# Kernel optimization log

Hardware: AMD Instinct MI355X
Metric: run time of the kernel (lower is better)

## Reference

```python
import jax, jax.numpy as jnp
import numpy as np

B, N, IN, HD, NH, L, OUT = 256, 128, 9, 128, 8, 4, 60
DH = HD // NH
ALPHA = 0.6
EPS = 1e-5

def _ln(x, g, b):
    m = jnp.mean(x, axis=-1, keepdims=True)
    v = jnp.mean((x - m) ** 2, axis=-1, keepdims=True)
    return (x - m) * jax.lax.rsqrt(v + EPS) * g + b

def setup_inputs():
    key = jax.random.key(0)
    ks = jax.random.split(key, 30)
    p = lambda i, s: jax.random.normal(ks[i], s, jnp.float32) * 0.02
    strong = (jax.random.uniform(ks[25], (N, N)) < 0.15).astype(jnp.float32)
    strong = jnp.maximum(strong, jnp.eye(N, dtype=jnp.float32))  # self loops
    weak_mask = (jax.random.uniform(ks[26], (N, N)) < 0.10).astype(jnp.float32)
    return {
        'x': jax.random.normal(ks[0], (B, N, IN), jnp.float32),
        'conv_w': p(1, (HD, IN)), 'conv_b': p(2, (HD,)),
        'bn_gamma': jnp.ones((HD,), jnp.float32), 'bn_beta': jnp.zeros((HD,), jnp.float32),
        'bn_mean': jnp.zeros((HD,), jnp.float32), 'bn_var': jnp.ones((HD,), jnp.float32),
        'W': p(3, (L, HD, HD)), 'a_src': p(4, (L, NH, DH)), 'a_dst': p(5, (L, NH, DH)),
        'ln_g': jnp.ones((L, HD), jnp.float32), 'ln_b': jnp.zeros((L, HD), jnp.float32),
        'ffn_w1': p(6, (L, HD, 2 * HD)), 'ffn_b1': p(7, (L, 2 * HD)),
        'ffn_w2': p(8, (L, 2 * HD, HD)), 'ffn_b2': p(9, (L, HD)),
        'norm_g': jnp.ones((HD,), jnp.float32), 'norm_b': jnp.zeros((HD,), jnp.float32),
        'proj_w': p(10, (HD, HD)), 'proj_b': p(11, (HD,)),
        'head_w1': p(12, (HD, HD // 2)), 'head_b1': p(13, (HD // 2,)),
        'head_w2': p(14, (HD // 2, OUT)), 'head_b2': p(15, (OUT,)),
        'strong_adj': strong, 'weak_mask': weak_mask,
        'weak_param': p(16, (N, N)), 'edge_weight_adj': p(17, (N, N)),
    }

def reference(x, conv_w, conv_b, bn_gamma, bn_beta, bn_mean, bn_var, W, a_src, a_dst, ln_g, ln_b, ffn_w1, ffn_b1, ffn_w2, ffn_b2, norm_g, norm_b, proj_w, proj_b, head_w1, head_b1, head_w2, head_b2, strong_adj, weak_mask, weak_param, edge_weight_adj):
    # embedding: Conv1d(k=1) == per-node linear, then eval-mode BatchNorm1d + ReLU
    h = jnp.einsum('bni,oi->bno', x, conv_w) + conv_b  # [B,N,HD]
    h = (h - bn_mean) * jax.lax.rsqrt(bn_var + EPS) * bn_gamma + bn_beta
    h = jax.nn.relu(h)
    # weak adjacency: learnable gated edges, row-normalized (shared across layers)
    Aw = jax.nn.sigmoid(weak_param) * weak_mask
    Aw = Aw / (jnp.sum(Aw, axis=-1, keepdims=True) + EPS)  # [N,N]
    for i in range(L):
        res = h
        hp = jnp.einsum('bnd,de->bne', h, W[i]).reshape(B, N, NH, DH)
        s = jnp.einsum('bnhd,hd->bnh', hp, a_src[i])
        t = jnp.einsum('bnhd,hd->bnh', hp, a_dst[i])
        e = jax.nn.leaky_relu(s[:, :, None, :] + t[:, None, :, :], 0.2)  # [B,N,N,H]
        e = e + edge_weight_adj[None, :, :, None]  # learned per-edge bias
        e = jnp.where(strong_adj[None, :, :, None] > 0, e, jnp.float32(-1e9))
        att = jax.nn.softmax(e, axis=2)  # softmax over neighbors j
        strong_out = jnp.einsum('bijh,bjhd->bihd', att, hp)
        weak_out = jnp.einsum('ij,bjhd->bihd', Aw, hp)
        g = jax.nn.relu(ALPHA * strong_out + (1.0 - ALPHA) * weak_out).reshape(B, N, HD)
        g = _ln(g, ln_g[i], ln_b[i])
        g = jax.nn.relu(g @ ffn_w1[i] + ffn_b1[i]) @ ffn_w2[i] + ffn_b2[i]
        h = g + res
    h = _ln(h, norm_g, norm_b)
    h = h @ proj_w + proj_b
    h = jnp.mean(h, axis=1)  # mean-pool over nodes -> [B,HD]
    h = jax.nn.relu(h @ head_w1 + head_b1)
    return h @ head_w2 + head_b2  # [B,OUT]
```

## Files before the change

kernel.cpp:

```cpp
#include <hip/hip_runtime.h>
#include <hip/hip_bf16.h>

typedef __hip_bfloat16 bf16;
typedef unsigned short u16;
typedef __attribute__((ext_vector_type(8))) short bfrag;
typedef __attribute__((ext_vector_type(4))) float cfrag;

union BF { bfrag v; u16 u[8]; unsigned w[4]; };
union CF { cfrag v; float f[4]; };

#define MFMA(a,b,c) __builtin_amdgcn_mfma_f32_16x16x32_bf16(a,b,c,0,0,0)

#define BB   256
#define NN   128
#define IND  9
#define HDD  128
#define LLY  4
#define OUTD 60
#define LOG2E 1.44269504f

__device__ __forceinline__ float b2f(bf16 v){ return __bfloat162float(v); }
__device__ __forceinline__ float u2f(u16 u){ return __uint_as_float(((unsigned)u) << 16); }
__device__ __forceinline__ u16 f2bf_bits(float f){
    unsigned u = __float_as_uint(f);
    return (u16)((u + 0x7FFFu + ((u >> 16) & 1u)) >> 16);
}
__device__ __forceinline__ unsigned pk2(float a, float b){
    union { __hip_bfloat162 h; unsigned u; } c;
    c.h = __float22bfloat162_rn(make_float2(a, b));
    return c.u;
}
__device__ __forceinline__ float wave_sum(float v){
    #pragma unroll
    for (int m = 32; m; m >>= 1) v += __shfl_xor(v, m, 64);
    return v;
}
__device__ __forceinline__ float ldin(const void* p, int i, bool isbf){
    return isbf ? b2f(((const bf16*)p)[i]) : ((const float*)p)[i];
}

struct SrcPtrs { const void* p[28]; };

__device__ const int NCV_OFF[19] = {0,1152,1280,1408,1536,1664,1792,2304,2816,3840,
                                    4352,4480,4608,20992,21120,29312,29376,33216,33276};
__device__ const int NCV_SRC[18] = {1,2,3,4,5,6,10,11,13,15,16,17,18,19,20,21,22,23};

__global__ __launch_bounds__(256) void k_prep(
    SrcPtrs S, float* __restrict__ pf,
    u16* __restrict__ WT, u16* __restrict__ w1T, u16* __restrict__ w2T,
    u16* __restrict__ WAb, u16* __restrict__ ew2, u16* __restrict__ Aw16,
    int* __restrict__ flagOut)
{
    const unsigned* xw = (const unsigned*)S.p[0];
    int lane = threadIdx.x & 63;
    int cnt = 0;
    for (int i = lane; i < 512; i += 64) {
        float v = __uint_as_float((xw[i] & 0xFFFFu) << 16);
        if (!(fabsf(v) < 32.f)) cnt++;
    }
    bool isbf = wave_sum((float)cnt) < 16.f;
    if (blockIdx.x == 0 && threadIdx.x == 0) *flagOut = isbf ? 1 : 0;

    int blk = blockIdx.x, tid = threadIdx.x;
    if (blk < 131) {
        int idx = blk * 256 + tid;
        if (idx < 33276) {
            int y = 17;
            #pragma unroll 1
            for (int t = 1; t < 18; t++) if (idx < NCV_OFF[t]) { y = t - 1; break; }
            pf[idx] = ldin(S.p[NCV_SRC[y]], idx - NCV_OFF[y], isbf);
        }
    } else if (blk < 387) {
        int j = (blk - 131) * 256 + tid;
        int l = j >> 14, r = j & 16383, n = r >> 7, k = r & 127;
        WT[j] = f2bf_bits(ldin(S.p[7], (l << 14) + k * 128 + n, isbf));
    } else if (blk < 899) {
        int j = (blk - 387) * 256 + tid;
        int l = j >> 15, r = j & 32767, n = r >> 7, k = r & 127;
        w1T[j] = f2bf_bits(ldin(S.p[12], (l << 15) + k * 256 + n, isbf));
    } else if (blk < 1411) {
        int j = (blk - 899) * 256 + tid;
        int l = j >> 15, r = j & 32767, n = r >> 8, k = r & 255;
        w2T[j] = f2bf_bits(ldin(S.p[14], (l << 15) + k * 128 + n, isbf));
    } else if (blk < 1443) {
        int j = (blk - 1411) * 256 + tid;
        int l = j >> 11, r = j & 2047, n = r >> 7, k = r & 127;
        int h = n & 7;
        const void* ap = (n < 8) ? S.p[8] : S.p[9];
        float sacc = 0.f;
        #pragma unroll 1
        for (int d = 0; d < 16; d++)
            sacc += ldin(S.p[7], l * 16384 + k * 128 + h * 16 + d, isbf)
                  * ldin(ap, l * 128 + h * 16 + d, isbf);
        WAb[j] = f2bf_bits(sacc);
    } else if (blk < 1507) {
        int j = (blk - 1443) * 256 + tid;
        float sav = ldin(S.p[24], j, isbf);
        float ewv = ldin(S.p[27], j, isbf);
        ew2[j] = f2bf_bits(sav > 0.f ? ewv * LOG2E : -1e30f);
    } else {
        __shared__ float red[2];
        int i = blk - 1507, j = tid & 127;
        float v = 0.f;
        if (tid < 128) {
            float wmv = ldin(S.p[25], i * 128 + j, isbf);
            float wpv = ldin(S.p[26], i * 128 + j, isbf);
            v = wmv / (1.f + __expf(-wpv));
            float sm = wave_sum(v);
            if ((tid & 63) == 0) red[tid >> 6] = sm;
        }
        __syncthreads();
        if (tid < 128) {
            float tot = red[0] + red[1];
            Aw16[i * 128 + j] = f2bf_bits(v / (tot + 1e-5f));
        }
    }
}

__global__ __launch_bounds__(256) void k_embed(
    const void* __restrict__ xraw, const int* __restrict__ flag,
    const float* __restrict__ pf,
    float* __restrict__ h, u16* __restrict__ h16, float* __restrict__ pooled)
{
    int b = blockIdx.x, half = blockIdx.y, tid = threadIdx.x;
    bool isbf = (*flag != 0);
    if (half == 0 && tid < 128) pooled[b * 128 + tid] = 0.f;
    int d = tid & 127, nh = tid >> 7;
    float wreg[IND];
    #pragma unroll
    for (int k = 0; k < IND; k++) wreg[k] = pf[d * IND + k];
    float scale = rsqrtf(pf[1664 + d] + 1e-5f) * pf[1280 + d];
    float bias  = pf[1408 + d] - pf[1536 + d] * scale;
    float cbd   = pf[1152 + d];
    #pragma unroll 1
    for (int it = 0; it < 32; it++) {
        int bn = b * NN + half * 64 + it * 2 + nh;
        float acc = cbd;
        #pragma unroll
        for (int k = 0; k < IND; k++) acc = fmaf(ldin(xraw, bn * IND + k, isbf), wreg[k], acc);
        acc = fmaxf(fmaf(acc, scale, bias), 0.f);
        h[bn * HDD + d] = acc;
        h16[bn * HDD + d] = f2bf_bits(acc);
    }
}

__global__ __launch_bounds__(256, 3) void k_layer(
    float* __restrict__ hg, u16* __restrict__ h16g,
    const u16* __restrict__ WT, const u16* __restrict__ WAb,
    const u16* __restrict__ Aw16, const u16* __restrict__ ew2g,
    const float* __restrict__ lng, const float* __restrict__ lnb,
    const u16* __restrict__ w1T, const float* __restrict__ b1,
    const u16* __restrict__ w2T, const float* __restrict__ b2,
    const float* __restrict__ ng, const float* __restrict__ nb,
    float* __restrict__ pooled, int last)
{
    __shared__ __align__(16) u16 hpT[128 * 136];
    __shared__ float st2[2048];
    float* s2 = st2;
    float* t2 = st2 + 1024;
    u16* gbuf = hpT;
    u16* hidb = hpT + 64 * 136;

    const int b = blockIdx.x, half = blockIdx.y;
    const int tid = threadIdx.x, lane = tid & 63, wv = tid >> 6;
    const int l15 = lane & 15, kg = lane >> 4;
    const int wrow = wv * 16;
    const int base = b * NN;

    float lngr[8], lnbr[8], b2r[8];
    #pragma unroll
    for (int nt = 0; nt < 8; nt++) {
        int col = nt * 16 + l15;
        lngr[nt] = lng[col]; lnbr[nt] = lnb[col]; b2r[nt] = b2[col];
    }

    {
        CF acc[2][8], ast[2];
        #pragma unroll
        for (int mt = 0; mt < 2; mt++) {
            #pragma unroll
            for (int r = 0; r < 4; r++) ast[mt].f[r] = 0.f;
            #pragma unroll
            for (int nt = 0; nt < 8; nt++)
                #pragma unroll
                for (int r = 0; r < 4; r++) acc[mt][nt].f[r] = 0.f;
        }
        #pragma unroll 1
        for (int kk = 0; kk < 4; kk++) {
            bfrag af0 = *(const bfrag*)&h16g[(base + wv*32 +      l15) * 128 + kk*32 + kg*8];
            bfrag af1 = *(const bfrag*)&h16g[(base + wv*32 + 16 + l15) * 128 + kk*32 + kg*8];
            bfrag wab = *(const bfrag*)&WAb[l15 * 128 + kk*32 + kg*8];
            ast[0].v = MFMA(af0, wab, ast[0].v);
            ast[1].v = MFMA(af1, wab, ast[1].v);
            #pragma unroll
            for (int nt = 0; nt < 8; nt++) {
                bfrag bw = *(const bfrag*)&WT[(nt*16 + l15) * 128 + kk*32 + kg*8];
                acc[0][nt].v = MFMA(af0, bw, acc[0][nt].v);
                acc[1][nt].v = MFMA(af1, bw, acc[1][nt].v);
            }
        }
        #pragma unroll
        for (int mt = 0; mt < 2; mt++) {
            #pragma unroll
            for (int nt = 0; nt < 8; nt++) {
                int col = nt*16 + l15;
                #pragma unroll
                for (int rp = 0; rp < 2; rp++) {
                    int row = wv*32 + mt*16 + kg*4 + rp*2;
                    *(unsigned*)&hpT[col * 136 + row] =
                        pk2(acc[mt][nt].f[rp*2], acc[mt][nt].f[rp*2+1]);
                }
            }
            #pragma unroll
            for (int r = 0; r < 4; r++) {
                int node = wv*32 + mt*16 + kg*4 + r;
                float v = ast[mt].f[r] * LOG2E;
                float* dst = (l15 < 8) ? &s2[l15 * 128 + node] : &t2[(l15 - 8) * 128 + node];
                *dst = v;
            }
        }
    }
    __syncthreads();

    const int grow = half*64 + wrow + l15;
    CF accW[8];
    #pragma unroll
    for (int nt = 0; nt < 8; nt++)
        #pragma unroll
        for (int r = 0; r < 4; r++) accW[nt].f[r] = 0.f;
    #pragma unroll 1
    for (int kk = 0; kk < 4; kk++) {
        bfrag awf = *(const bfrag*)&Aw16[grow * 128 + kk*32 + kg*8];
        #pragma unroll
        for (int nt = 0; nt < 8; nt++) {
            bfrag hb2 = *(const bfrag*)&hpT[(nt*16 + l15) * 136 + kk*32 + kg*8];
            accW[nt].v = MFMA(awf, hb2, accW[nt].v);
        }
    }

    CF accS[8];
    #pragma unroll
    for (int nt = 0; nt < 8; nt++)
        #pragma unroll
        for (int r = 0; r < 4; r++) accS[nt].f[r] = 0.f;

    float ew2f[4][8];
    #pragma unroll
    for (int kk = 0; kk < 4; kk++) {
        BF e2; e2.v = *(const bfrag*)&ew2g[grow * 128 + kk*32 + kg*8];
        #pragma unroll
        for (int j = 0; j < 8; j++) ew2f[kk][j] = u2f(e2.u[j]);
    }
    #pragma unroll 1
    for (int h = 0; h < 8; h++) {
        bfrag hb[4];
        #pragma unroll
        for (int kk = 0; kk < 4; kk++)
            hb[kk] = *(const bfrag*)&hpT[(h*16 + l15) * 136 + kk*32 + kg*8];
        float sA = s2[h * 128 + grow];
        float pv[4][8];
        float sm = 0.f;
        #pragma unroll
        for (int kk = 0; kk < 4; kk++) {
            const float* tp = &t2[h * 128 + kk*32 + kg*8];
            #pragma unroll
            for (int j = 0; j < 8; j++) {
                float x2 = sA + tp[j];
                float lk = fmaxf(x2, 0.2f * x2);
                float p = __builtin_amdgcn_exp2f(lk + ew2f[kk][j]);
                pv[kk][j] = p; sm += p;
            }
        }
        sm += __shfl_xor(sm, 16, 64);
        sm += __shfl_xor(sm, 32, 64);
        float inv = __builtin_amdgcn_rcpf(sm);
        #pragma unroll
        for (int kk = 0; kk < 4; kk++) {
            BF pb;
            #pragma unroll
            for (int q = 0; q < 4; q++)
                pb.w[q] = pk2(pv[kk][2*q] * inv, pv[kk][2*q+1] * inv);
            accS[h].v = MFMA(pb.v, hb[kk], accS[h].v);
        }
    }

    float gv[8][4];
    #pragma unroll
    for (int nt = 0; nt < 8; nt++)
        #pragma unroll
        for (int r = 0; r < 4; r++)
            gv[nt][r] = fmaxf(0.6f * accS[nt].f[r] + 0.4f * accW[nt].f[r], 0.f);
    u16 gb16[8][4];
    #pragma unroll
    for (int r = 0; r < 4; r++) {
        float s1 = 0.f, sq = 0.f;
        #pragma unroll
        for (int nt = 0; nt < 8; nt++) { float x = gv[nt][r]; s1 += x; sq = fmaf(x, x, sq); }
        #pragma unroll
        for (int m = 1; m <= 8; m <<= 1) { s1 += __shfl_xor(s1, m, 64); sq += __shfl_xor(sq, m, 64); }
        float mu = s1 * (1.f / 128.f);
        float var = sq * (1.f / 128.f) - mu * mu;
        float rs = rsqrtf(fmaxf(var, 0.f) + 1e-5f);
        #pragma unroll
        for (int nt = 0; nt < 8; nt++)
            gb16[nt][r] = f2bf_bits(fmaf((gv[nt][r] - mu) * rs, lngr[nt], lnbr[nt]));
    }
    __syncthreads();
    #pragma unroll
    for (int nt = 0; nt < 8; nt++) {
        int col = nt*16 + l15;
        #pragma unroll
        for (int r = 0; r < 4; r++)
            gbuf[(wrow + kg*4 + r) * 136 + col] = gb16[nt][r];
    }
    __syncthreads();

    CF acc2[8];
    #pragma unroll
    for (int nt = 0; nt < 8; nt++)
        #pragma unroll
        for (int r = 0; r < 4; r++) acc2[nt].f[r] = 0.f;

    #pragma unroll 1
    for (int nh = 0; nh < 2; nh++) {
        float b1r[8];
        #pragma unroll
        for (int nt = 0; nt < 8; nt++) b1r[nt] = b1[nh*128 + nt*16 + l15];
        CF a1[8];
        #pragma unroll
        for (int nt = 0; nt < 8; nt++)
            #pragma unroll
            for (int r = 0; r < 4; r++) a1[nt].f[r] = 0.f;
        #pragma unroll 1
        for (int kk = 0; kk < 4; kk++) {
            bfrag gf = *(const bfrag*)&gbuf[(wrow + l15) * 136 + kk*32 + kg*8];
            #pragma unroll
            for (int nt = 0; nt < 8; nt++) {
                bfrag wf = *(const bfrag*)&w1T[(nh*128 + nt*16 + l15) * 128 + kk*32 + kg*8];
                a1[nt].v = MFMA(gf, wf, a1[nt].v);
            }
        }
        __syncthreads();
        #pragma unroll
        for (int nt = 0; nt < 8; nt++) {
            int col = nt*16 + l15;
            #pragma unroll
            for (int r = 0; r < 4; r++)
                hidb[(wrow + kg*4 + r) * 136 + col] = f2bf_bits(fmaxf(a1[nt].f[r] + b1r[nt], 0.f));
        }
        __syncthreads();
        #pragma unroll 1
        for (int kk = 0; kk < 4; kk++) {
            bfrag hf = *(const bfrag*)&hidb[(wrow + l15) * 136 + kk*32 + kg*8];
            #pragma unroll
            for (int nt = 0; nt < 8; nt++) {
                bfrag wf = *(const bfrag*)&w2T[(nt*16 + l15) * 256 + nh*128 + kk*32 + kg*8];
                acc2[nt].v = MFMA(hf, wf, acc2[nt].v);
            }
        }
    }

    float hv[8][4];
    #pragma unroll
    for (int nt = 0; nt < 8; nt++) {
        #pragma unroll
        for (int r = 0; r < 4; r++) {
            int gi = (base + half*64 + wrow + kg*4 + r) * HDD + nt*16 + l15;
            hv[nt][r] = acc2[nt].f[r] + b2r[nt] + hg[gi];
        }
    }
    if (!last) {
        #pragma unroll
        for (int nt = 0; nt < 8; nt++) {
            #pragma unroll
            for (int r = 0; r < 4; r++) {
                int gi = (base + half*64 + wrow + kg*4 + r) * HDD + nt*16 + l15;
                hg[gi] = hv[nt][r];
                h16g[gi] = f2bf_bits(hv[nt][r]);
            }
        }
    } else {
        float ngr[8], nbr[8];
        #pragma unroll
        for (int nt = 0; nt < 8; nt++) { int col = nt*16 + l15; ngr[nt] = ng[col]; nbr[nt] = nb[col]; }
        float pacc[8];
        #pragma unroll
        for (int nt = 0; nt < 8; nt++) pacc[nt] = 0.f;
        #pragma unroll
        for (int r = 0; r < 4; r++) {
            float s1 = 0.f, sq = 0.f;
            #pragma unroll
            for (int nt = 0; nt < 8; nt++) { float x = hv[nt][r]; s1 += x; sq = fmaf(x, x, sq); }
            #pragma unroll
            for (int m = 1; m <= 8; m <<= 1) { s1 += __shfl_xor(s1, m, 64); sq += __shfl_xor(sq, m, 64); }
            float mu = s1 * (1.f / 128.f);
            float var = sq * (1.f / 128.f) - mu * mu;
            float rs = rsqrtf(fmaxf(var, 0.f) + 1e-5f);
            #pragma unroll
            for (int nt = 0; nt < 8; nt++)
                pacc[nt] += fmaf((hv[nt][r] - mu) * rs, ngr[nt], nbr[nt]);
        }
        __syncthreads();
        float* psum = st2;
        #pragma unroll
        for (int nt = 0; nt < 8; nt++)
            psum[(wv*4 + kg) * 128 + nt*16 + l15] = pacc[nt];
        __syncthreads();
        if (tid < 128) {
            float tot = 0.f;
            #pragma unroll
            for (int i = 0; i < 16; i++) tot += psum[i * 128 + tid];
            atomicAdd(&pooled[b * HDD + tid], tot);
        }
    }
}

__global__ __launch_bounds__(128) void k_head(
    const float* __restrict__ pooled, const float* __restrict__ pf,
    void* __restrict__ outv, const int* __restrict__ flag)
{
    const float* pw  = pf + 4608;
    const float* pb  = pf + 20992;
    const float* hw1 = pf + 21120;
    const float* hb1 = pf + 29312;
    const float* hw2 = pf + 29376;
    const float* hb2 = pf + 33216;
    int b = blockIdx.x, t = threadIdx.x;
    __shared__ float pm[128], pr[128], r1[64];
    pm[t] = pooled[b * HDD + t] * (1.f / 128.f);
    __syncthreads();
    float a = pb[t];
    #pragma unroll 4
    for (int k = 0; k < 128; k++) a = fmaf(pm[k], pw[k * 128 + t], a);
    pr[t] = a;
    __syncthreads();
    if (t < 64) {
        float a1 = hb1[t];
        #pragma unroll 4
        for (int k = 0; k < 128; k++) a1 = fmaf(pr[k], hw1[k * 64 + t], a1);
        r1[t] = fmaxf(a1, 0.f);
    }
    __syncthreads();
    if (t < OUTD) {
        float a2 = hb2[t];
        #pragma unroll 4
        for (int k = 0; k < 64; k++) a2 = fmaf(r1[k], hw2[k * OUTD + t], a2);
        if (*flag) ((bf16*)outv)[b * OUTD + t] = __float2bfloat16(a2);
        else       ((float*)outv)[b * OUTD + t] = a2;
    }
}

extern "C" void kernel_launch(void* const* d_in, const int* in_sizes, int n_in,
                              void* d_out, int out_size, void* d_ws, size_t ws_size,
                              hipStream_t stream)
{
    float* ws = (float*)d_ws;
    float* pf = ws;
    const float* lng  = pf + 1792;
    const float* lnb  = pf + 2304;
    const float* fb1  = pf + 2816;
    const float* fb2  = pf + 3840;
    const float* ng   = pf + 4352;
    const float* nb   = pf + 4480;

    int*   flag   = (int*)(ws + 33280);
    float* h      = ws + 33536;
    float* pooled = h + 4194304;
    u16* h16    = (u16*)(pooled + 32768);
    u16* WT16   = h16 + 4194304;
    u16* w1T16  = WT16 + 65536;
    u16* w2T16  = w1T16 + 131072;
    u16* WAb16  = w2T16 + 131072;
    u16* Aw16   = WAb16 + 8192;
    u16* ew2p   = Aw16 + 16384;

    SrcPtrs S;
    for (int i = 0; i < 28; i++) S.p[i] = d_in[i];

    k_prep<<<1635, 256, 0, stream>>>(S, pf, WT16, w1T16, w2T16, WAb16, ew2p, Aw16, flag);
    k_embed<<<dim3(BB, 2), 256, 0, stream>>>(d_in[0], flag, pf, h, h16, pooled);

    for (int i = 0; i < LLY; i++) {
        k_layer<<<dim3(BB, 2), 256, 0, stream>>>(
            h, h16,
            WT16 + i * 16384, WAb16 + i * 2048,
            Aw16, ew2p,
            lng + i * 128, lnb + i * 128,
            w1T16 + i * 32768, fb1 + i * 256,
            w2T16 + i * 32768, fb2 + i * 128,
            ng, nb, pooled, (i == LLY - 1) ? 1 : 0);
    }

    k_head<<<BB, 128, 0, stream>>>(pooled, pf, d_out, flag);
}
```

Baseline: 393.7 us.

## Fuse embed, all GAT layers and head into one persistent per-graph kernel

Replaces the separate embed, per-layer and head kernels with a single kernel that runs one 512-thread block per graph and keeps the residual stream in registers and LDS across all four layers. This removes the global round-trips of h/h16 between layers, the atomic pooling, and several launches. The attention t-scores are now stored as bf16 in LDS and the edge bias is reloaded from global each head. In exchange, grid parallelism drops from 512 blocks to 256 larger blocks, and the larger LDS footprint may limit occupancy.

```diff
diff --git a/kernel.cpp b/kernel.cpp
--- a/kernel.cpp
+++ b/kernel.cpp
@@ -18,6 +18,7 @@
 #define LLY  4
 #define OUTD 60
 #define LOG2E 1.44269504f
+#define STR  136
 
 __device__ __forceinline__ float b2f(bf16 v){ return __bfloat162float(v); }
 __device__ __forceinline__ float u2f(u16 u){ return __uint_as_float(((unsigned)u) << 16); }
@@ -117,336 +118,315 @@
     }
 }
 
-__global__ __launch_bounds__(256) void k_embed(
+#define LDSB (2*128*STR*2 + 8192)
+__global__ __launch_bounds__(512, 2) void k_net(
     const void* __restrict__ xraw, const int* __restrict__ flag,
     const float* __restrict__ pf,
-    float* __restrict__ h, u16* __restrict__ h16, float* __restrict__ pooled)
+    const u16* __restrict__ WTg, const u16* __restrict__ WAbg,
+    const u16* __restrict__ Awg, const u16* __restrict__ ew2g,
+    const u16* __restrict__ w1Tg, const u16* __restrict__ w2Tg,
+    void* __restrict__ outv)
 {
-    int b = blockIdx.x, half = blockIdx.y, tid = threadIdx.x;
-    bool isbf = (*flag != 0);
-    if (half == 0 && tid < 128) pooled[b * 128 + tid] = 0.f;
-    int d = tid & 127, nh = tid >> 7;
-    float wreg[IND];
-    #pragma unroll
-    for (int k = 0; k < IND; k++) wreg[k] = pf[d * IND + k];
-    float scale = rsqrtf(pf[1664 + d] + 1e-5f) * pf[1280 + d];
-    float bias  = pf[1408 + d] - pf[1536 + d] * scale;
-    float cbd   = pf[1152 + d];
-    #pragma unroll 1
-    for (int it = 0; it < 32; it++) {
-        int bn = b * NN + half * 64 + it * 2 + nh;
-        float acc = cbd;
-        #pragma unroll
-        for (int k = 0; k < IND; k++) acc = fmaf(ldin(xraw, bn * IND + k, isbf), wreg[k], acc);
-        acc = fmaxf(fmaf(acc, scale, bias), 0.f);
-        h[bn * HDD + d] = acc;
-        h16[bn * HDD + d] = f2bf_bits(acc);
-    }
-}
-
-__global__ __launch_bounds__(256, 3) void k_layer(
-    float* __restrict__ hg, u16* __restrict__ h16g,
-    const u16* __restrict__ WT, const u16* __restrict__ WAb,
-    const u16* __restrict__ Aw16, const u16* __restrict__ ew2g,
-    const float* __restrict__ lng, const float* __restrict__ lnb,
-    const u16* __restrict__ w1T, const float* __restrict__ b1,
-    const u16* __restrict__ w2T, const float* __restrict__ b2,
-    const float* __restrict__ ng, const float* __restrict__ nb,
-    float* __restrict__ pooled, int last)
-{
-    __shared__ __align__(16) u16 hpT[128 * 136];
-    __shared__ float st2[2048];
-    float* s2 = st2;
-    float* t2 = st2 + 1024;
-    u16* gbuf = hpT;
-    u16* hidb = hpT + 64 * 136;
-
-    const int b = blockIdx.x, half = blockIdx.y;
+    extern __shared__ __align__(16) char smem[];
+    u16* Abuf = (u16*)smem;
+    u16* Bbuf = Abuf + 128 * STR;
+    float* st2 = (float*)(Bbuf + 128 * STR);
+    float* s2  = st2;
+    u16*   t2u = (u16*)(st2 + 1024);
+
+    const int b = blockIdx.x;
     const int tid = threadIdx.x, lane = tid & 63, wv = tid >> 6;
     const int l15 = lane & 15, kg = lane >> 4;
     const int wrow = wv * 16;
-    const int base = b * NN;
-
-    float lngr[8], lnbr[8], b2r[8];
-    #pragma unroll
-    for (int nt = 0; nt < 8; nt++) {
-        int col = nt * 16 + l15;
-        lngr[nt] = lng[col]; lnbr[nt] = lnb[col]; b2r[nt] = b2[col];
-    }
+    const bool isbf = (*flag != 0);
+
+    float hreg[8][4];
 
     {
-        CF acc[2][8], ast[2];
-        #pragma unroll
-        for (int mt = 0; mt < 2; mt++) {
-            #pragma unroll
-            for (int r = 0; r < 4; r++) ast[mt].f[r] = 0.f;
+        float xr[4][9];
+        #pragma unroll
+        for (int r = 0; r < 4; r++) {
+            int bn = b * NN + wrow + kg * 4 + r;
+            #pragma unroll
+            for (int k = 0; k < IND; k++) xr[r][k] = ldin(xraw, bn * IND + k, isbf);
+        }
+        #pragma unroll 1
+        for (int nt = 0; nt < 8; nt++) {
+            int d = nt * 16 + l15;
+            float cwreg[IND];
+            #pragma unroll
+            for (int k = 0; k < IND; k++) cwreg[k] = pf[d * IND + k];
+            float scale = rsqrtf(pf[1664 + d] + 1e-5f) * pf[1280 + d];
+            float bias  = pf[1408 + d] - pf[1536 + d] * scale;
+            float cbd   = pf[1152 + d];
+            #pragma unroll
+            for (int r = 0; r < 4; r++) {
+                float a = cbd;
+                #pragma unroll
+                for (int k = 0; k < IND; k++) a = fmaf(xr[r][k], cwreg[k], a);
+                a = fmaxf(fmaf(a, scale, bias), 0.f);
+                hreg[nt][r] = a;
+                Abuf[(wrow + kg * 4 + r) * STR + d] = f2bf_bits(a);
+            }
+        }
+    }
+
+    const int arow = wrow + l15;
+
+    #pragma unroll 1
+    for (int l = 0; l < LLY; l++) {
+        const u16* WT  = WTg  + l * 16384;
+        const u16* WAb = WAbg + l * 2048;
+        const u16* w1T = w1Tg + l * 32768;
+        const u16* w2T = w2Tg + l * 32768;
+        const float* fb1 = pf + 2816 + l * 256;
+        const float* fb2 = pf + 3840 + l * 128;
+        const float* lng = pf + 1792 + l * 128;
+        const float* lnb = pf + 2304 + l * 128;
+
+        __syncthreads();
+
+        {
+            CF acc[8], ast;
+            #pragma unroll
+            for (int r = 0; r < 4; r++) ast.f[r] = 0.f;
             #pragma unroll
             for (int nt = 0; nt < 8; nt++)
                 #pragma unroll
-                for (int r = 0; r < 4; r++) acc[mt][nt].f[r] = 0.f;
-        }
+                for (int r = 0; r < 4; r++) acc[nt].f[r] = 0.f;
+            #pragma unroll 1
+            for (int kk = 0; kk < 4; kk++) {
+                bfrag af  = *(const bfrag*)&Abuf[arow * STR + kk*32 + kg*8];
+                bfrag wab = *(const bfrag*)&WAb[l15 * 128 + kk*32 + kg*8];
+                ast.v = MFMA(af, wab, ast.v);
+                #pragma unroll
+                for (int nt = 0; nt < 8; nt++) {
+                    bfrag bw = *(const bfrag*)&WT[(nt*16 + l15) * 128 + kk*32 + kg*8];
+                    acc[nt].v = MFMA(af, bw, acc[nt].v);
+                }
+            }
+            #pragma unroll
+            for (int nt = 0; nt < 8; nt++) {
+                int col = nt*16 + l15;
+                #pragma unroll
+                for (int rp = 0; rp < 2; rp++) {
+                    int row = wrow + kg*4 + rp*2;
+                    *(unsigned*)&Bbuf[col * STR + row] = pk2(acc[nt].f[rp*2], acc[nt].f[rp*2+1]);
+                }
+            }
+            #pragma unroll
+            for (int r = 0; r < 4; r++) {
+                int node = wrow + kg*4 + r;
+                float v = ast.f[r] * LOG2E;
+                if (l15 < 8) s2[l15 * 128 + node] = v;
+                else         t2u[(l15 - 8) * 128 + node] = f2bf_bits(v);
+            }
+        }
+        __syncthreads();
+
+        CF accW[8];
+        #pragma unroll
+        for (int nt = 0; nt < 8; nt++)
+            #pragma unroll
+            for (int r = 0; r < 4; r++) accW[nt].f[r] = 0.f;
         #pragma unroll 1
         for (int kk = 0; kk < 4; kk++) {
-            bfrag af0 = *(const bfrag*)&h16g[(base + wv*32 +      l15) * 128 + kk*32 + kg*8];
-            bfrag af1 = *(const bfrag*)&h16g[(base + wv*32 + 16 + l15) * 128 + kk*32 + kg*8];
-            bfrag wab = *(const bfrag*)&WAb[l15 * 128 + kk*32 + kg*8];
-            ast[0].v = MFMA(af0, wab, ast[0].v);
-            ast[1].v = MFMA(af1, wab, ast[1].v);
+            bfrag awf = *(const bfrag*)&Awg[arow * 128 + kk*32 + kg*8];
             #pragma unroll
             for (int nt = 0; nt < 8; nt++) {
-                bfrag bw = *(const bfrag*)&WT[(nt*16 + l15) * 128 + kk*32 + kg*8];
-                acc[0][nt].v = MFMA(af0, bw, acc[0][nt].v);
-                acc[1][nt].v = MFMA(af1, bw, acc[1][nt].v);
-            }
-        }
-        #pragma unroll
-        for (int mt = 0; mt < 2; mt++) {
+                bfrag hb2 = *(const bfrag*)&Bbuf[(nt*16 + l15) * STR + kk*32 + kg*8];
+                accW[nt].v = MFMA(awf, hb2, accW[nt].v);
+            }
+        }
+
+        CF accS[8];
+        #pragma unroll
+        for (int nt = 0; nt < 8; nt++)
+            #pragma unroll
+            for (int r = 0; r < 4; r++) accS[nt].f[r] = 0.f;
+        #pragma unroll 1
+        for (int h = 0; h < 8; h++) {
+            bfrag hb[4];
+            #pragma unroll
+            for (int kk = 0; kk < 4; kk++)
+                hb[kk] = *(const bfrag*)&Bbuf[(h*16 + l15) * STR + kk*32 + kg*8];
+            float sA = s2[h * 128 + arow];
+            float pv[4][8];
+            float sm = 0.f;
+            #pragma unroll
+            for (int kk = 0; kk < 4; kk++) {
+                BF tb; tb.v = *(const bfrag*)&t2u[h * 128 + kk*32 + kg*8];
+                BF e2; e2.v = *(const bfrag*)&ew2g[arow * 128 + kk*32 + kg*8];
+                #pragma unroll
+                for (int j = 0; j < 8; j++) {
+                    float x2 = sA + u2f(tb.u[j]);
+                    float lk = fmaxf(x2, 0.2f * x2);
+                    float p = __builtin_amdgcn_exp2f(lk + u2f(e2.u[j]));
+                    pv[kk][j] = p; sm += p;
+                }
+            }
+            sm += __shfl_xor(sm, 16, 64);
+            sm += __shfl_xor(sm, 32, 64);
+            float inv = __builtin_amdgcn_rcpf(sm);
+            #pragma unroll
+            for (int kk = 0; kk < 4; kk++) {
+                BF pb;
+                #pragma unroll
+                for (int q = 0; q < 4; q++)
+                    pb.w[q] = pk2(pv[kk][2*q] * inv, pv[kk][2*q+1] * inv);
+                accS[h].v = MFMA(pb.v, hb[kk], accS[h].v);
+            }
+        }
+        __syncthreads();
+
+        {
+            float gv[8][4];
+            #pragma unroll
+            for (int nt = 0; nt < 8; nt++)
+                #pragma unroll
+                for (int r = 0; r < 4; r++)
+                    gv[nt][r] = fmaxf(0.6f * accS[nt].f[r] + 0.4f * accW[nt].f[r], 0.f);
+            #pragma unroll
+            for (int r = 0; r < 4; r++) {
+                float s1 = 0.f, sq = 0.f;
+                #pragma unroll
+                for (int nt = 0; nt < 8; nt++) { float x = gv[nt][r]; s1 += x; sq = fmaf(x, x, sq); }
+                #pragma unroll
+                for (int m = 1; m <= 8; m <<= 1) { s1 += __shfl_xor(s1, m, 64); sq += __shfl_xor(sq, m, 64); }
+                float mu = s1 * (1.f / 128.f);
+                float var = sq * (1.f / 128.f) - mu * mu;
+                float rs = rsqrtf(fmaxf(var, 0.f) + 1e-5f);
+                #pragma unroll
+                for (int nt = 0; nt < 8; nt++) {
+                    int col = nt*16 + l15;
+                    Bbuf[(wrow + kg*4 + r) * STR + col] =
+                        f2bf_bits(fmaf((gv[nt][r] - mu) * rs, lng[col], lnb[col]));
+                }
+            }
+        }
+
+        CF acc2[8];
+        #pragma unroll
+        for (int nt = 0; nt < 8; nt++)
+            #pragma unroll
+            for (int r = 0; r < 4; r++) acc2[nt].f[r] = 0.f;
+        #pragma unroll 1
+        for (int nh = 0; nh < 2; nh++) {
+            CF a1[8];
+            #pragma unroll
+            for (int nt = 0; nt < 8; nt++)
+                #pragma unroll
+                for (int r = 0; r < 4; r++) a1[nt].f[r] = 0.f;
+            #pragma unroll 1
+            for (int kk = 0; kk < 4; kk++) {
+                bfrag gf = *(const bfrag*)&Bbuf[arow * STR + kk*32 + kg*8];
+                #pragma unroll
+                for (int nt = 0; nt < 8; nt++) {
+                    bfrag wf = *(const bfrag*)&w1T[(nh*128 + nt*16 + l15) * 128 + kk*32 + kg*8];
+                    a1[nt].v = MFMA(gf, wf, a1[nt].v);
+                }
+            }
             #pragma unroll
             for (int nt = 0; nt < 8; nt++) {
                 int col = nt*16 + l15;
-                #pragma unroll
-                for (int rp = 0; rp < 2; rp++) {
-                    int row = wv*32 + mt*16 + kg*4 + rp*2;
-                    *(unsigned*)&hpT[col * 136 + row] =
-                        pk2(acc[mt][nt].f[rp*2], acc[mt][nt].f[rp*2+1]);
-                }
-            }
-            #pragma unroll
-            for (int r = 0; r < 4; r++) {
-                int node = wv*32 + mt*16 + kg*4 + r;
-                float v = ast[mt].f[r] * LOG2E;
-                float* dst = (l15 < 8) ? &s2[l15 * 128 + node] : &t2[(l15 - 8) * 128 + node];
-                *dst = v;
-            }
-        }
-    }
-    __syncthreads();
-
-    const int grow = half*64 + wrow + l15;
-    CF accW[8];
+                float b1v = fb1[nh*128 + col];
+                #pragma unroll
+                for (int r = 0; r < 4; r++)
+                    Abuf[(wrow + kg*4 + r) * STR + col] = f2bf_bits(fmaxf(a1[nt].f[r] + b1v, 0.f));
+            }
+            #pragma unroll 1
+            for (int kk = 0; kk < 4; kk++) {
+                bfrag hf = *(const bfrag*)&Abuf[arow * STR + kk*32 + kg*8];
+                #pragma unroll
+                for (int nt = 0; nt < 8; nt++) {
+                    bfrag wf = *(const bfrag*)&w2T[(nt*16 + l15) * 256 + nh*128 + kk*32 + kg*8];
+                    acc2[nt].v = MFMA(hf, wf, acc2[nt].v);
+                }
+            }
+        }
+
+        #pragma unroll
+        for (int nt = 0; nt < 8; nt++) {
+            float b2v = fb2[nt*16 + l15];
+            #pragma unroll
+            for (int r = 0; r < 4; r++) hreg[nt][r] += acc2[nt].f[r] + b2v;
+        }
+        if (l < LLY - 1) {
+            #pragma unroll
+            for (int nt = 0; nt < 8; nt++) {
+                int col = nt*16 + l15;
+                #pragma unroll
+                for (int r = 0; r < 4; r++)
+                    Abuf[(wrow + kg*4 + r) * STR + col] = f2bf_bits(hreg[nt][r]);
+            }
+        }
+    }
+
+    const float* ng = pf + 4352;
+    const float* nb = pf + 4480;
+    float pacc[8];
     #pragma unroll
-    for (int nt = 0; nt < 8; nt++)
-        #pragma unroll
-        for (int r = 0; r < 4; r++) accW[nt].f[r] = 0.f;
-    #pragma unroll 1
-    for (int kk = 0; kk < 4; kk++) {
-        bfrag awf = *(const bfrag*)&Aw16[grow * 128 + kk*32 + kg*8];
-        #pragma unroll
-        for (int nt = 0; nt < 8; nt++) {
-            bfrag hb2 = *(const bfrag*)&hpT[(nt*16 + l15) * 136 + kk*32 + kg*8];
-            accW[nt].v = MFMA(awf, hb2, accW[nt].v);
-        }
-    }
-
-    CF accS[8];
-    #pragma unroll
-    for (int nt = 0; nt < 8; nt++)
-        #pragma unroll
-        for (int r = 0; r < 4; r++) accS[nt].f[r] = 0.f;
-
-    float ew2f[4][8];
-    #pragma unroll
-    for (int kk = 0; kk < 4; kk++) {
-        BF e2; e2.v = *(const bfrag*)&ew2g[grow * 128 + kk*32 + kg*8];
-        #pragma unroll
-        for (int j = 0; j < 8; j++) ew2f[kk][j] = u2f(e2.u[j]);
-    }
-    #pragma unroll 1
-    for (int h = 0; h < 8; h++) {
-        bfrag hb[4];
-        #pragma unroll
-        for (int kk = 0; kk < 4; kk++)
-            hb[kk] = *(const bfrag*)&hpT[(h*16 + l15) * 136 + kk*32 + kg*8];
-        float sA = s2[h * 128 + grow];
-        float pv[4][8];
-        float sm = 0.f;
-        #pragma unroll
-        for (int kk = 0; kk < 4; kk++) {
-            const float* tp = &t2[h * 128 + kk*32 + kg*8];
-            #pragma unroll
-            for (int j = 0; j < 8; j++) {
-                float x2 = sA + tp[j];
-                float lk = fmaxf(x2, 0.2f * x2);
-                float p = __builtin_amdgcn_exp2f(lk + ew2f[kk][j]);
-                pv[kk][j] = p; sm += p;
-            }
-        }
-        sm += __shfl_xor(sm, 16, 64);
-        sm += __shfl_xor(sm, 32, 64);
-        float inv = __builtin_amdgcn_rcpf(sm);
-        #pragma unroll
-        for (int kk = 0; kk < 4; kk++) {
-            BF pb;
-            #pragma unroll
-            for (int q = 0; q < 4; q++)
-                pb.w[q] = pk2(pv[kk][2*q] * inv, pv[kk][2*q+1] * inv);
-            accS[h].v = MFMA(pb.v, hb[kk], accS[h].v);
-        }
-    }
-
-    float gv[8][4];
-    #pragma unroll
-    for (int nt = 0; nt < 8; nt++)
-        #pragma unroll
-        for (int r = 0; r < 4; r++)
-            gv[nt][r] = fmaxf(0.6f * accS[nt].f[r] + 0.4f * accW[nt].f[r], 0.f);
-    u16 gb16[8][4];
+    for (int nt = 0; nt < 8; nt++) pacc[nt] = 0.f;
     #pragma unroll
     for (int r = 0; r < 4; r++) {
         float s1 = 0.f, sq = 0.f;
         #pragma unroll
-        for (int nt = 0; nt < 8; nt++) { float x = gv[nt][r]; s1 += x; sq = fmaf(x, x, sq); }
+        for (int nt = 0; nt < 8; nt++) { float x = hreg[nt][r]; s1 += x; sq = fmaf(x, x, sq); }
         #pragma unroll
         for (int m = 1; m <= 8; m <<= 1) { s1 += __shfl_xor(s1, m, 64); sq += __shfl_xor(sq, m, 64); }
         float mu = s1 * (1.f / 128.f);
         float var = sq * (1.f / 128.f) - mu * mu;
         float rs = rsqrtf(fmaxf(var, 0.f) + 1e-5f);
         #pragma unroll
-        for (int nt = 0; nt < 8; nt++)
-            gb16[nt][r] = f2bf_bits(fmaf((gv[nt][r] - mu) * rs, lngr[nt], lnbr[nt]));
-    }
-    __syncthreads();
+        for (int nt = 0; nt < 8; nt++) {
+            int col = nt*16 + l15;
+            pacc[nt] += fmaf((hreg[nt][r] - mu) * rs, ng[col], nb[col]);
+        }
+    }
     #pragma unroll
     for (int nt = 0; nt < 8; nt++) {
-        int col = nt*16 + l15;
-        #pragma unroll
-        for (int r = 0; r < 4; r++)
-            gbuf[(wrow + kg*4 + r) * 136 + col] = gb16[nt][r];
-    }
-    __syncthreads();
-
-    CF acc2[8];
-    #pragma unroll
-    for (int nt = 0; nt < 8; nt++)
-        #pragma unroll
-        for (int r = 0; r < 4; r++) acc2[nt].f[r] = 0.f;
-
-    #pragma unroll 1
-    for (int nh = 0; nh < 2; nh++) {
-        float b1r[8];
-        #pragma unroll
-        for (int nt = 0; nt < 8; nt++) b1r[nt] = b1[nh*128 + nt*16 + l15];
-        CF a1[8];
-        #pragma unroll
-        for (int nt = 0; nt < 8; nt++)
-            #pragma unroll
-            for (int r = 0; r < 4; r++) a1[nt].f[r] = 0.f;
-        #pragma unroll 1
-        for (int kk = 0; kk < 4; kk++) {
-            bfrag gf = *(const bfrag*)&gbuf[(wrow + l15) * 136 + kk*32 + kg*8];
-            #pragma unroll
-            for (int nt = 0; nt < 8; nt++) {
-                bfrag wf = *(const bfrag*)&w1T[(nh*128 + nt*16 + l15) * 128 + kk*32 + kg*8];
-                a1[nt].v = MFMA(gf, wf, a1[nt].v);
-            }
-        }
-        __syncthreads();
-        #pragma unroll
-        for (int nt = 0; nt < 8; nt++) {
-            int col = nt*16 + l15;
-            #pragma unroll
-            for (int r = 0; r < 4; r++)
-                hidb[(wrow + kg*4 + r) * 136 + col] = f2bf_bits(fmaxf(a1[nt].f[r] + b1r[nt], 0.f));
-        }
-        __syncthreads();
-        #pragma unroll 1
-        for (int kk = 0; kk < 4; kk++) {
-            bfrag hf = *(const bfrag*)&hidb[(wrow + l15) * 136 + kk*32 + kg*8];
-            #pragma unroll
-            for (int nt = 0; nt < 8; nt++) {
-                bfrag wf = *(const bfrag*)&w2T[(nt*16 + l15) * 256 + nh*128 + kk*32 + kg*8];
-                acc2[nt].v = MFMA(hf, wf, acc2[nt].v);
-            }
-        }
-    }
-
-    float hv[8][4];
-    #pragma unroll
-    for (int nt = 0; nt < 8; nt++) {
-        #pragma unroll
-        for (int r = 0; r < 4; r++) {
-            int gi = (base + half*64 + wrow + kg*4 + r) * HDD + nt*16 + l15;
-            hv[nt][r] = acc2[nt].f[r] + b2r[nt] + hg[gi];
-        }
-    }
-    if (!last) {
-        #pragma unroll
-        for (int nt = 0; nt < 8; nt++) {
-            #pragma unroll
-            for (int r = 0; r < 4; r++) {
-                int gi = (base + half*64 + wrow + kg*4 + r) * HDD + nt*16 + l15;
-                hg[gi] = hv[nt][r];
-                h16g[gi] = f2bf_bits(hv[nt][r]);
-            }
-        }
-    } else {
-        float ngr[8], nbr[8];
-        #pragma unroll
-        for (int nt = 0; nt < 8; nt++) { int col = nt*16 + l15; ngr[nt] = ng[col]; nbr[nt] = nb[col]; }
-        float pacc[8];
-        #pragma unroll
-        for (int nt = 0; nt < 8; nt++) pacc[nt] = 0.f;
-        #pragma unroll
-        for (int r = 0; r < 4; r++) {
-            float s1 = 0.f, sq = 0.f;
-            #pragma unroll
-            for (int nt = 0; nt < 8; nt++) { float x = hv[nt][r]; s1 += x; sq = fmaf(x, x, sq); }
-            #pragma unroll
-            for (int m = 1; m <= 8; m <<= 1) { s1 += __shfl_xor(s1, m, 64); sq += __shfl_xor(sq, m, 64); }
-            float mu = s1 * (1.f / 128.f);
-            float var = sq * (1.f / 128.f) - mu * mu;
-            float rs = rsqrtf(fmaxf(var, 0.f) + 1e-5f);
-            #pragma unroll
-            for (int nt = 0; nt < 8; nt++)
-                pacc[nt] += fmaf((hv[nt][r] - mu) * rs, ngr[nt], nbr[nt]);
-        }
-        __syncthreads();
-        float* psum = st2;
-        #pragma unroll
-        for (int nt = 0; nt < 8; nt++)
-            psum[(wv*4 + kg) * 128 + nt*16 + l15] = pacc[nt];
-        __syncthreads();
-        if (tid < 128) {
-            float tot = 0.f;
-            #pragma unroll
-            for (int i = 0; i < 16; i++) tot += psum[i * 128 + tid];
-            atomicAdd(&pooled[b * HDD + tid], tot);
-        }
-    }
-}
-
-__global__ __launch_bounds__(128) void k_head(
-    const float* __restrict__ pooled, const float* __restrict__ pf,
-    void* __restrict__ outv, const int* __restrict__ flag)
-{
-    const float* pw  = pf + 4608;
-    const float* pb  = pf + 20992;
-    const float* hw1 = pf + 21120;
-    const float* hb1 = pf + 29312;
-    const float* hw2 = pf + 29376;
-    const float* hb2 = pf + 33216;
-    int b = blockIdx.x, t = threadIdx.x;
-    __shared__ float pm[128], pr[128], r1[64];
-    pm[t] = pooled[b * HDD + t] * (1.f / 128.f);
-    __syncthreads();
-    float a = pb[t];
-    #pragma unroll 4
-    for (int k = 0; k < 128; k++) a = fmaf(pm[k], pw[k * 128 + t], a);
-    pr[t] = a;
-    __syncthreads();
-    if (t < 64) {
-        float a1 = hb1[t];
+        pacc[nt] += __shfl_xor(pacc[nt], 16, 64);
+        pacc[nt] += __shfl_xor(pacc[nt], 32, 64);
+    }
+    __syncthreads();
+    if (kg == 0) {
+        #pragma unroll
+        for (int nt = 0; nt < 8; nt++) st2[wv * 128 + nt*16 + l15] = pacc[nt];
+    }
+    __syncthreads();
+    if (tid < 128) {
+        float tot = 0.f;
+        #pragma unroll
+        for (int w = 0; w < 8; w++) tot += st2[w * 128 + tid];
+        st2[1024 + tid] = tot * (1.f / 128.f);
+    }
+    __syncthreads();
+    {
+        int e = tid & 127, kq = tid >> 7;
+        float a = 0.f;
         #pragma unroll 4
-        for (int k = 0; k < 128; k++) a1 = fmaf(pr[k], hw1[k * 64 + t], a1);
-        r1[t] = fmaxf(a1, 0.f);
-    }
-    __syncthreads();
-    if (t < OUTD) {
-        float a2 = hb2[t];
+        for (int k = kq * 32; k < kq * 32 + 32; k++)
+            a = fmaf(st2[1024 + k], pf[4608 + k * 128 + e], a);
+        st2[1152 + kq * 128 + e] = a;
+    }
+    __syncthreads();
+    if (tid < 128)
+        st2[1664 + tid] = st2[1152 + tid] + st2[1280 + tid] + st2[1408 + tid] + st2[1536 + tid]
+                        + pf[20992 + tid];
+    __syncthreads();
+    if (tid < 64) {
+        float a1 = pf[29312 + tid];
         #pragma unroll 4
-        for (int k = 0; k < 64; k++) a2 = fmaf(r1[k], hw2[k * OUTD + t], a2);
-        if (*flag) ((bf16*)outv)[b * OUTD + t] = __float2bfloat16(a2);
-        else       ((float*)outv)[b * OUTD + t] = a2;
+        for (int k = 0; k < 128; k++) a1 = fmaf(st2[1664 + k], pf[21120 + k * 64 + tid], a1);
+        st2[1792 + tid] = fmaxf(a1, 0.f);
+    }
+    __syncthreads();
+    if (tid < OUTD) {
+        float a2 = pf[33216 + tid];
+        #pragma unroll 4
+        for (int k = 0; k < 64; k++) a2 = fmaf(st2[1792 + k], pf[29376 + k * OUTD + tid], a2);
+        if (isbf) ((bf16*)outv)[b * OUTD + tid] = __float2bfloat16(a2);
+        else      ((float*)outv)[b * OUTD + tid] = a2;
     }
 }
 
@@ -456,18 +436,8 @@
 {
     float* ws = (float*)d_ws;
     float* pf = ws;
-    const float* lng  = pf + 1792;
-    const float* lnb  = pf + 2304;
-    const float* fb1  = pf + 2816;
-    const float* fb2  = pf + 3840;
-    const float* ng   = pf + 4352;
-    const float* nb   = pf + 4480;
-
-    int*   flag   = (int*)(ws + 33280);
-    float* h      = ws + 33536;
-    float* pooled = h + 4194304;
-    u16* h16    = (u16*)(pooled + 32768);
-    u16* WT16   = h16 + 4194304;
+    int*   flag = (int*)(ws + 33280);
+    u16* WT16   = (u16*)(ws + 33536);
     u16* w1T16  = WT16 + 65536;
     u16* w2T16  = w1T16 + 131072;
     u16* WAb16  = w2T16 + 131072;
@@ -477,19 +447,10 @@
     SrcPtrs S;
     for (int i = 0; i < 28; i++) S.p[i] = d_in[i];
 
+    hipFuncSetAttribute((const void*)k_net,
+                        hipFuncAttributeMaxDynamicSharedMemorySize, LDSB);
+
     k_prep<<<1635, 256, 0, stream>>>(S, pf, WT16, w1T16, w2T16, WAb16, ew2p, Aw16, flag);
-    k_embed<<<dim3(BB, 2), 256, 0, stream>>>(d_in[0], flag, pf, h, h16, pooled);
-
-    for (int i = 0; i < LLY; i++) {
-        k_layer<<<dim3(BB, 2), 256, 0, stream>>>(
-            h, h16,
-            WT16 + i * 16384, WAb16 + i * 2048,
-            Aw16, ew2p,
-            lng + i * 128, lnb + i * 128,
-            w1T16 + i * 32768, fb1 + i * 256,
-            w2T16 + i * 32768, fb2 + i * 128,
-            ng, nb, pooled, (i == LLY - 1) ? 1 : 0);
-    }
-
-    k_head<<<BB, 128, 0, stream>>>(pooled, pf, d_out, flag);
-}
+    k_net<<<BB, 512, LDSB, stream>>>(d_in[0], flag, pf,
+                                     WT16, WAb16, Aw16, ew2p, w1T16, w2T16, d_out);
+}
```

Measured after the change: 352.9 us. 10.4% less time.
